# Optimization experiments

Measured on AMD Instinct MI355X. Metric: run time of the kernel, lower is better.

The kernel has to match this reference:

```python
import jax, jax.numpy as jnp
import numpy as np
import math

B, L, D_MODEL, H = 2, 2048, 2048, 16
HD = D_MODEL // H  # 128


def _rope(x):
    # x: (B,H,L,HD) interleaved-pair RoPE (GPT-NeoX / RoFormer style with ::2 strides)
    hd = x.shape[-1]
    inv_freq = 1.0 / (10000.0 ** (jnp.arange(0, hd, 2, dtype=jnp.float32) / hd))  # (HD/2,)
    t = jnp.arange(x.shape[2], dtype=jnp.float32)
    freqs = t[:, None] * inv_freq[None, :]            # (L, HD/2)
    cos = jnp.cos(freqs)[None, None]                  # (1,1,L,HD/2)
    sin = jnp.sin(freqs)[None, None]
    x1 = x[..., ::2]
    x2 = x[..., 1::2]
    even = x1 * cos - x2 * sin
    odd = x1 * sin + x2 * cos
    # interleave even/odd back: (...,HD/2,2) -> (...,HD)
    return jnp.stack([even, odd], axis=-1).reshape(x.shape)


def setup_inputs() -> dict:
    key = jax.random.key(0)
    k1, k2, k3, k4, k5, k6 = jax.random.split(key, 6)
    x_q = jax.random.normal(k1, (B, L, D_MODEL), dtype=jnp.float32)
    x_kv = jax.random.normal(k2, (B, L, D_MODEL), dtype=jnp.float32)
    # causal additive mask: 0 keep, -1e9 masked, broadcastable to (B,H,L,S)
    causal = jnp.tril(jnp.ones((L, L), dtype=bool))
    attn_mask = jnp.where(causal, 0.0, -1e9).astype(jnp.float32)[None, None]
    s = 0.02
    w_q = jax.random.normal(k3, (D_MODEL, D_MODEL), dtype=jnp.float32) * s
    w_k = jax.random.normal(k4, (D_MODEL, D_MODEL), dtype=jnp.float32) * s
    w_v = jax.random.normal(k5, (D_MODEL, D_MODEL), dtype=jnp.float32) * s
    w_o = jax.random.normal(k6, (D_MODEL, D_MODEL), dtype=jnp.float32) * s
    return {"x_q": x_q, "x_kv": x_kv, "attn_mask": attn_mask,
            "w_q": w_q, "w_k": w_k, "w_v": w_v, "w_o": w_o}


def _shape(x):
    b, l, _ = x.shape
    return x.reshape(b, l, H, HD).transpose(0, 2, 1, 3)  # (B,H,L,HD)


def reference(x_q, x_kv, attn_mask, w_q, w_k, w_v, w_o):
    # torch Linear (no bias): y = x @ W.T
    q = _shape(x_q @ w_q.T)
    k = _shape(x_kv @ w_k.T)
    v = _shape(x_kv @ w_v.T)
    q = _rope(q)
    k = _rope(k)
    scale = 1.0 / math.sqrt(HD)
    scores = jnp.einsum('bhld,bhsd->bhls', q, k) * scale + attn_mask
    attn = jax.nn.softmax(scores, axis=-1)            # (B,H,L,S)
    out = jnp.einsum('bhls,bhsd->bhld', attn, v)
    out = out.transpose(0, 2, 1, 3).reshape(x_q.shape[0], x_q.shape[1], H * HD)
    out = out @ w_o.T
    return (out, attn)
```

## Files before the change

kernel.cpp:

```cpp
#include <hip/hip_runtime.h>
#include <hip/hip_bf16.h>
#include <math.h>

#define B_ 2
#define L_ 2048
#define D_ 2048
#define H_ 16
#define HD_ 128
#define E_ (B_*L_*D_)
#define W_ (D_*D_)

typedef __bf16 bf16;
typedef __bf16 bf16x8 __attribute__((ext_vector_type(8)));
typedef __bf16 bf16x4 __attribute__((ext_vector_type(4)));
typedef float  f32x4  __attribute__((ext_vector_type(4)));

#define GLL16(gp_, lp_) __builtin_amdgcn_global_load_lds( \
    (const __attribute__((address_space(1))) void*)(gp_), \
    (__attribute__((address_space(3))) void*)(lp_), 16, 0, 0)

#define BARRIER() do { asm volatile("" ::: "memory"); \
    __builtin_amdgcn_s_barrier(); \
    asm volatile("" ::: "memory"); } while (0)

#define WAITN(N) asm volatile("s_waitcnt vmcnt(" #N ")" ::: "memory")
#define LGKM0SB() do { asm volatile("s_waitcnt lgkmcnt(0)" ::: "memory"); \
    __builtin_amdgcn_sched_barrier(0); } while (0)

__global__ void prep(const float* __restrict__ xq, const float* __restrict__ xkv,
                     const float* __restrict__ wq, const float* __restrict__ wk,
                     const float* __restrict__ wv, const float* __restrict__ wo,
                     bf16* __restrict__ xqb, bf16* __restrict__ xkvb,
                     bf16* __restrict__ wqb, bf16* __restrict__ wkb,
                     bf16* __restrict__ wvb, bf16* __restrict__ wob,
                     float* __restrict__ ct, float* __restrict__ st) {
  int g = blockIdx.x;
  if (g < 16384) {
    const float* s = (g < 8192) ? xq : xkv;
    bf16* d = (g < 8192) ? xqb : xkvb;
    int i = ((g & 8191) * 256 + threadIdx.x) * 4;
    f32x4 v = *reinterpret_cast<const f32x4*>(s + i);
    bf16x4 o; o[0]=(bf16)v[0]; o[1]=(bf16)v[1]; o[2]=(bf16)v[2]; o[3]=(bf16)v[3];
    *reinterpret_cast<bf16x4*>(d + i) = o;
  } else if (g < 32768) {
    int gg = g - 16384;
    int which = gg >> 12;
    const float* s = (which==0)?wq:(which==1)?wk:(which==2)?wv:wo;
    bf16* d = (which==0)?wqb:(which==1)?wkb:(which==2)?wvb:wob;
    int i = ((gg & 4095) * 256 + threadIdx.x) * 4;
    f32x4 v = *reinterpret_cast<const f32x4*>(s + i);
    bf16x4 o; o[0]=(bf16)v[0]; o[1]=(bf16)v[1]; o[2]=(bf16)v[2]; o[3]=(bf16)v[3];
    *reinterpret_cast<bf16x4*>(d + i) = o;
  } else {
    int idx = (g - 32768) * 256 + threadIdx.x;
    int t = idx >> 6, i = idx & 63;
    float inv = powf(10000.0f, -2.0f * (float)i / 128.0f);
    float f = (float)t * inv;
    ct[t * 64 + i] = cosf(f);
    st[t * 64 + i] = sinf(f);
  }
}

__global__ __launch_bounds__(512, 2) void gemm_qkv256(
    const bf16* __restrict__ xq, const bf16* __restrict__ xkv,
    const bf16* __restrict__ wq, const bf16* __restrict__ wk, const bf16* __restrict__ wv,
    const float* __restrict__ ct, const float* __restrict__ st,
    bf16* __restrict__ Qo, bf16* __restrict__ Ko, bf16* __restrict__ Vt) {
  __shared__ bf16 Ab[2][256 * 64];
  __shared__ bf16 Bb[2][256 * 64];
  const int tid = threadIdx.x;
  const int w = tid >> 6, lane = tid & 63;
  const int l15 = lane & 15, lg = lane >> 4;
  const int wm = w >> 2, wn = w & 3;
  const int which = blockIdx.x >> 3;
  const int n0 = (blockIdx.x & 7) * 256;
  const int m0 = blockIdx.y * 256;
  const bf16* A  = (which == 0) ? xq : xkv;
  const bf16* Wt = (which == 0) ? wq : ((which == 1) ? wk : wv);

  int rS[4], cS[4];
#pragma unroll
  for (int s = 0; s < 4; ++s) {
    int ch = s * 512 + tid;
    rS[s] = ch >> 3;
    cS[s] = ((ch & 7) ^ ((ch >> 3) & 7)) << 3;
  }

  auto stage = [&](int t, int buf) {
#pragma unroll
    for (int s = 0; s < 4; ++s) {
      GLL16(A  + (size_t)(m0 + rS[s]) * D_ + t * 64 + cS[s], &Ab[buf][0] + s * 4096 + w * 512);
      GLL16(Wt + (size_t)(n0 + rS[s]) * D_ + t * 64 + cS[s], &Bb[buf][0] + s * 4096 + w * 512);
    }
  };
#define RD(bufp, row, x) (*reinterpret_cast<const bf16x8*>((bufp) + (row) * 64 + (((x) ^ (l15 & 7)) << 3)))

  f32x4 acc[8][4];
#pragma unroll
  for (int i = 0; i < 8; ++i)
#pragma unroll
    for (int n = 0; n < 4; ++n) acc[i][n] = (f32x4){0.f, 0.f, 0.f, 0.f};

  stage(0, 0);
  WAITN(0);
  BARRIER();

  for (int t = 0; t < 32; ++t) {
    const bf16* Al = &Ab[t & 1][0];
    const bf16* Bl = &Bb[t & 1][0];
    bf16x8 af[4], bfr[4];
    const bool hn = (t + 1 < 32);

    if (hn) stage(t + 1, (t & 1) ^ 1);
#pragma unroll
    for (int n = 0; n < 4; ++n) bfr[n] = RD(Bl, wn * 64 + n * 16 + l15, lg);
#pragma unroll
    for (int i = 0; i < 4; ++i) af[i] = RD(Al, wm * 128 + i * 16 + l15, lg);
    BARRIER(); LGKM0SB();
    __builtin_amdgcn_s_setprio(1);
#pragma unroll
    for (int i = 0; i < 4; ++i)
#pragma unroll
      for (int n = 0; n < 4; ++n)
        acc[i][n] = __builtin_amdgcn_mfma_f32_16x16x32_bf16(af[i], bfr[n], acc[i][n], 0, 0, 0);
    __builtin_amdgcn_s_setprio(0);
    BARRIER();

#pragma unroll
    for (int i = 0; i < 4; ++i) af[i] = RD(Al, wm * 128 + (4 + i) * 16 + l15, lg);
    BARRIER(); LGKM0SB();
    __builtin_amdgcn_s_setprio(1);
#pragma unroll
    for (int i = 0; i < 4; ++i)
#pragma unroll
      for (int n = 0; n < 4; ++n)
        acc[4 + i][n] = __builtin_amdgcn_mfma_f32_16x16x32_bf16(af[i], bfr[n], acc[4 + i][n], 0, 0, 0);
    __builtin_amdgcn_s_setprio(0);
    BARRIER();

#pragma unroll
    for (int n = 0; n < 4; ++n) bfr[n] = RD(Bl, wn * 64 + n * 16 + l15, 4 + lg);
#pragma unroll
    for (int i = 0; i < 4; ++i) af[i] = RD(Al, wm * 128 + i * 16 + l15, 4 + lg);
    BARRIER(); LGKM0SB();
    __builtin_amdgcn_s_setprio(1);
#pragma unroll
    for (int i = 0; i < 4; ++i)
#pragma unroll
      for (int n = 0; n < 4; ++n)
        acc[i][n] = __builtin_amdgcn_mfma_f32_16x16x32_bf16(af[i], bfr[n], acc[i][n], 0, 0, 0);
    __builtin_amdgcn_s_setprio(0);
    BARRIER();

#pragma unroll
    for (int i = 0; i < 4; ++i) af[i] = RD(Al, wm * 128 + (4 + i) * 16 + l15, 4 + lg);
    BARRIER(); LGKM0SB();
    __builtin_amdgcn_s_setprio(1);
#pragma unroll
    for (int i = 0; i < 4; ++i)
#pragma unroll
      for (int n = 0; n < 4; ++n)
        acc[4 + i][n] = __builtin_amdgcn_mfma_f32_16x16x32_bf16(af[i], bfr[n], acc[4 + i][n], 0, 0, 0);
    __builtin_amdgcn_s_setprio(0);
    if (hn) WAITN(0);
    BARRIER();
  }
#undef RD

  if (which == 2) {
    const int b = m0 >> 11;
#pragma unroll
    for (int mi = 0; mi < 8; ++mi) {
      int row = m0 + wm * 128 + mi * 16 + lg * 4;
      int l = row & 2047;
#pragma unroll
      for (int ni = 0; ni < 4; ++ni) {
        int c = n0 + wn * 64 + ni * 16 + l15;
        int hd = (b * 16 + (c >> 7)) * 128 + (c & 127);
        bf16x4 o;
        o[0] = (bf16)acc[mi][ni][0]; o[1] = (bf16)acc[mi][ni][1];
        o[2] = (bf16)acc[mi][ni][2]; o[3] = (bf16)acc[mi][ni][3];
        *reinterpret_cast<bf16x4*>(Vt + (size_t)hd * L_ + l) = o;
      }
    }
  } else {
    bf16* Out = which ? Ko : Qo;
    const bool odd = (l15 & 1);
#pragma unroll
    for (int mi = 0; mi < 8; ++mi) {
      int row = m0 + wm * 128 + mi * 16 + lg * 4;
      int l = row & 2047;
#pragma unroll
      for (int ni = 0; ni < 4; ++ni) {
        int c = n0 + wn * 64 + ni * 16 + l15;
        int i = (c & 127) >> 1;
#pragma unroll
        for (int r = 0; r < 4; ++r) {
          float own = acc[mi][ni][r];
          float prt = __shfl_xor(own, 1, 64);
          float cc = ct[(size_t)(l + r) * 64 + i];
          float ss = st[(size_t)(l + r) * 64 + i];
          float res = odd ? (prt * ss + own * cc) : (own * cc - prt * ss);
          Out[(size_t)(row + r) * D_ + c] = (bf16)res;
        }
      }
    }
  }
}

__global__ __launch_bounds__(256, 4) void gemm_bt(const bf16* __restrict__ A,
                                                  const bf16* __restrict__ Bw,
                                                  float* __restrict__ Cout,
                                                  int M, int N, int K) {
  __shared__ bf16 As[128 * 64];
  __shared__ bf16 Bs[128 * 64];
  const int tid = threadIdx.x;
  const int lane = tid & 63;
  const int w = tid >> 6;
  const int l15 = lane & 15, lg = lane >> 4;
  const int m0 = blockIdx.y * 128, n0 = blockIdx.x * 128;
  const int wm = (w >> 1) * 64, wn = (w & 1) * 64;

  int rowS[4], schS[4];
#pragma unroll
  for (int s = 0; s < 4; ++s) {
    int cl = s * 256 + tid;
    rowS[s] = cl >> 3;
    schS[s] = ((cl & 7) ^ ((cl >> 3) & 7)) << 3;
  }

  f32x4 acc[4][4];
#pragma unroll
  for (int m = 0; m < 4; ++m)
#pragma unroll
    for (int n = 0; n < 4; ++n) acc[m][n] = (f32x4){0.f, 0.f, 0.f, 0.f};

  for (int kt = 0; kt < K; kt += 64) {
    __syncthreads();
#pragma unroll
    for (int s = 0; s < 4; ++s) {
      GLL16(A  + (size_t)(m0 + rowS[s]) * K + kt + schS[s], As + s * 2048 + w * 512);
      GLL16(Bw + (size_t)(n0 + rowS[s]) * K + kt + schS[s], Bs + s * 2048 + w * 512);
    }
    __syncthreads();
#pragma unroll
    for (int kk = 0; kk < 64; kk += 32) {
      bf16x8 af[4], bfr[4];
#pragma unroll
      for (int m = 0; m < 4; ++m)
        af[m] = *reinterpret_cast<const bf16x8*>(
            As + (wm + m * 16 + l15) * 64 + ((((kk >> 3) + lg) ^ (l15 & 7)) << 3));
#pragma unroll
      for (int n = 0; n < 4; ++n)
        bfr[n] = *reinterpret_cast<const bf16x8*>(
            Bs + (wn + n * 16 + l15) * 64 + ((((kk >> 3) + lg) ^ (l15 & 7)) << 3));
#pragma unroll
      for (int m = 0; m < 4; ++m)
#pragma unroll
        for (int n = 0; n < 4; ++n)
          acc[m][n] = __builtin_amdgcn_mfma_f32_16x16x32_bf16(af[m], bfr[n], acc[m][n], 0, 0, 0);
    }
  }
#pragma unroll
  for (int m = 0; m < 4; ++m) {
    int orow = m0 + wm + m * 16 + lg * 4;
#pragma unroll
    for (int n = 0; n < 4; ++n) {
      int col = n0 + wn + n * 16 + l15;
#pragma unroll
      for (int r = 0; r < 4; ++r)
        Cout[(size_t)(orow + r) * N + col] = acc[m][n][r];
    }
  }
}

__global__ __launch_bounds__(256, 2) void attn_fused(const bf16* __restrict__ Qb,
                                                     const bf16* __restrict__ Kb,
                                                     const bf16* __restrict__ Vt,
                                                     float* __restrict__ attn,
                                                     bf16* __restrict__ Oh) {
  __shared__ bf16 Klds[2][64 * 128];
  __shared__ bf16 Vlds[128 * 64];
  __shared__ bf16 Plds[4][32][72];

  const int tid = threadIdx.x;
  const int w = tid >> 6, lane = tid & 63;
  const int l15 = lane & 15, lg = lane >> 4;

  int g = blockIdx.x + 16 * blockIdx.y;
  int tq, bh;
  if (g < 256) { tq = g & 15;  bh = g >> 4; }
  else { int h2 = g - 256; tq = 15 - (h2 & 15); bh = 16 + (h2 >> 4); }
  const int b = bh >> 4, h = bh & 15;

  const int q0w = tq * 128 + w * 32;
  const int ntW = (q0w >> 6) + 1;
  const int ntB = 2 * tq + 2;
  const float sc2 = 0.08838834764831845f * 1.44269504088896f;

  const bf16* kb = Kb + ((size_t)b * L_) * D_ + h * HD_;
  const bf16* vb = Vt + (size_t)bh * HD_ * L_;
  float* arow = attn + ((size_t)bh * L_ + q0w) * L_;

  bf16x8 qf[2][4];
#pragma unroll
  for (int qc = 0; qc < 2; ++qc) {
    const bf16* qrow = Qb + ((size_t)b * L_ + q0w + qc * 16 + l15) * D_ + h * HD_;
#pragma unroll
    for (int c = 0; c < 4; ++c)
      qf[qc][c] = *reinterpret_cast<const bf16x8*>(qrow + c * 32 + lg * 8);
  }

  int rK[4], sK[4], rV[4], sV[4];
#pragma unroll
  for (int s = 0; s < 4; ++s) {
    int ck = s * 256 + tid;
    rK[s] = ck >> 4; sK[s] = ((ck & 15) ^ (rK[s] & 7)) << 3;
    rV[s] = ck >> 3; sV[s] = ((ck & 7) ^ (rV[s] & 7)) << 3;
  }

  auto stageK = [&](int gp, int buf) {
#pragma unroll
    for (int s = 0; s < 4; ++s)
      GLL16(kb + (size_t)(gp * 64 + rK[s]) * D_ + sK[s],
            &Klds[0][0] + buf * 8192 + s * 2048 + w * 512);
  };
  auto stageV = [&](int gp) {
#pragma unroll
    for (int s = 0; s < 4; ++s)
      GLL16(vb + (size_t)rV[s] * L_ + gp * 64 + sV[s],
            Vlds + s * 2048 + w * 512);
  };
  auto qkt = [&](const bf16* kl, f32x4 acc[2][4]) {
#pragma unroll
    for (int c = 0; c < 4; ++c)
#pragma unroll
      for (int t = 0; t < 4; ++t) {
        bf16x8 kf = *reinterpret_cast<const bf16x8*>(
            kl + (t * 16 + l15) * 128 + ((((c << 2) + lg) ^ (l15 & 7)) << 3));
#pragma unroll
        for (int qc = 0; qc < 2; ++qc)
          acc[qc][t] = __builtin_amdgcn_mfma_f32_16x16x32_bf16(qf[qc][c], kf, acc[qc][t], 0, 0, 0);
      }
  };
  auto zstore32 = [&](int gp) {
#pragma unroll
    for (int qc = 0; qc < 2; ++qc)
#pragma unroll
      for (int t = 0; t < 4; ++t)
#pragma unroll
        for (int r = 0; r < 4; ++r)
          arow[(size_t)(qc * 16 + lg * 4 + r) * L_ + gp * 64 + t * 16 + l15] = 0.f;
  };

  float sum[2][4] = {{0.f,0.f,0.f,0.f},{0.f,0.f,0.f,0.f}};
  stageK(0, 0);
  for (int gp = 0; gp < ntB; ++gp) {
    BARRIER();
    const bool hn = (gp + 1 < ntB);
    if (hn) { stageK(gp + 1, (gp + 1) & 1); WAITN(4); }
    else    { WAITN(0); }
    BARRIER();
    if (gp < ntW) {
      f32x4 acc[2][4];
#pragma unroll
      for (int qc = 0; qc < 2; ++qc)
#pragma unroll
        for (int t = 0; t < 4; ++t) acc[qc][t] = (f32x4){0.f,0.f,0.f,0.f};
      qkt(&Klds[gp & 1][0], acc);
      if (gp < ntW - 1) {
#pragma unroll
        for (int qc = 0; qc < 2; ++qc)
#pragma unroll
          for (int t = 0; t < 4; ++t)
#pragma unroll
            for (int r = 0; r < 4; ++r)
              sum[qc][r] += exp2f(acc[qc][t][r] * sc2);
      } else {
#pragma unroll
        for (int qc = 0; qc < 2; ++qc)
#pragma unroll
          for (int t = 0; t < 4; ++t)
#pragma unroll
            for (int r = 0; r < 4; ++r) {
              int kc = gp * 64 + t * 16 + l15;
              int qr = q0w + qc * 16 + lg * 4 + r;
              sum[qc][r] += (kc <= qr) ? exp2f(acc[qc][t][r] * sc2) : 0.f;
            }
      }
    } else {
      zstore32(gp);
    }
  }
  float rinv[2][4];
#pragma unroll
  for (int qc = 0; qc < 2; ++qc)
#pragma unroll
    for (int r = 0; r < 4; ++r) {
      float s = sum[qc][r];
#pragma unroll
      for (int sh = 1; sh < 16; sh <<= 1)
        s += __shfl_xor(s, sh, 64);
      rinv[qc][r] = 1.0f / s;
    }

  f32x4 oacc[2][8];
#pragma unroll
  for (int qc = 0; qc < 2; ++qc)
#pragma unroll
    for (int i = 0; i < 8; ++i) oacc[qc][i] = (f32x4){0.f, 0.f, 0.f, 0.f};

  BARRIER();
  stageK(0, 0);
  for (int gp = 0; gp < ntB; ++gp) {
    BARRIER();
    stageV(gp);
    const bool hn = (gp + 1 < ntB);
    if (hn) stageK(gp + 1, (gp + 1) & 1);
    if (gp == 0) { WAITN(8); }
    else if (hn) { WAITN(40); }
    else         { WAITN(36); }
    BARRIER();
    const bool act = gp < ntW;
    float pv[2][4][4];
    if (act) {
      f32x4 acc[2][4];
#pragma unroll
      for (int qc = 0; qc < 2; ++qc)
#pragma unroll
        for (int t = 0; t < 4; ++t) acc[qc][t] = (f32x4){0.f,0.f,0.f,0.f};
      qkt(&Klds[gp & 1][0], acc);
      if (gp < ntW - 1) {
#pragma unroll
        for (int qc = 0; qc < 2; ++qc)
#pragma unroll
          for (int t = 0; t < 4; ++t)
#pragma unroll
            for (int r = 0; r < 4; ++r)
              pv[qc][t][r] = exp2f(acc[qc][t][r] * sc2) * rinv[qc][r];
      } else {
#pragma unroll
        for (int qc = 0; qc < 2; ++qc)
#pragma unroll
          for (int t = 0; t < 4; ++t)
#pragma unroll
            for (int r = 0; r < 4; ++r) {
              int kc = gp * 64 + t * 16 + l15;
              int qr = q0w + qc * 16 + lg * 4 + r;
              pv[qc][t][r] = (kc <= qr) ? exp2f(acc[qc][t][r] * sc2) * rinv[qc][r] : 0.f;
            }
      }
#pragma unroll
      for (int qc = 0; qc < 2; ++qc)
#pragma unroll
        for (int t = 0; t < 4; ++t)
#pragma unroll
          for (int r = 0; r < 4; ++r)
            Plds[w][qc * 16 + lg * 4 + r][t * 16 + l15] = (bf16)pv[qc][t][r];
    }
    if (hn) WAITN(4); else WAITN(0);
    if (act) {
#pragma unroll
      for (int qc = 0; qc < 2; ++qc)
#pragma unroll
        for (int t = 0; t < 4; ++t)
#pragma unroll
          for (int r = 0; r < 4; ++r)
            arow[(size_t)(qc * 16 + lg * 4 + r) * L_ + gp * 64 + t * 16 + l15] = pv[qc][t][r];
    } else {
      zstore32(gp);
    }
    BARRIER();
    if (act) {
      asm volatile("s_waitcnt lgkmcnt(0)" ::: "memory");
      __builtin_amdgcn_sched_barrier(0);
      bf16x8 pa[2][2];
#pragma unroll
      for (int qc = 0; qc < 2; ++qc)
#pragma unroll
        for (int ck = 0; ck < 2; ++ck)
          pa[qc][ck] = *reinterpret_cast<const bf16x8*>(&Plds[w][qc * 16 + l15][ck * 32 + lg * 8]);
#pragma unroll
      for (int ck = 0; ck < 2; ++ck)
#pragma unroll
        for (int t8 = 0; t8 < 8; ++t8) {
          bf16x8 vf = *reinterpret_cast<const bf16x8*>(
              Vlds + (t8 * 16 + l15) * 64 + ((((ck << 2) + lg) ^ (l15 & 7)) << 3));
#pragma unroll
          for (int qc = 0; qc < 2; ++qc)
            oacc[qc][t8] = __builtin_amdgcn_mfma_f32_16x16x32_bf16(pa[qc][ck], vf, oacc[qc][t8], 0, 0, 0);
        }
      asm volatile("s_waitcnt lgkmcnt(0)" ::: "memory");
    }
  }

  for (int gp2 = ntB; gp2 < 32; ++gp2) {
#pragma unroll
    for (int i = 0; i < 8; ++i)
      *reinterpret_cast<f32x4*>(arow + (size_t)(i * 4 + lg) * L_ + gp2 * 64 + l15 * 4)
          = (f32x4){0.f, 0.f, 0.f, 0.f};
  }

#pragma unroll
  for (int qc = 0; qc < 2; ++qc) {
    bf16* orow = Oh + ((size_t)b * L_ + q0w + qc * 16) * D_ + h * HD_;
#pragma unroll
    for (int t8 = 0; t8 < 8; ++t8)
#pragma unroll
      for (int r = 0; r < 4; ++r)
        orow[(size_t)(lg * 4 + r) * D_ + t8 * 16 + l15] = (bf16)oacc[qc][t8][r];
  }
}

extern "C" void kernel_launch(void* const* d_in, const int* in_sizes, int n_in,
                              void* d_out, int out_size, void* d_ws, size_t ws_size,
                              hipStream_t stream) {
  const float* x_q  = (const float*)d_in[0];
  const float* x_kv = (const float*)d_in[1];
  const float* w_q = (const float*)d_in[3];
  const float* w_k = (const float*)d_in[4];
  const float* w_v = (const float*)d_in[5];
  const float* w_o = (const float*)d_in[6];

  char* p = (char*)d_ws;
  auto alloc = [&](size_t bytes) { char* r = p; p += (bytes + 255) & ~(size_t)255; return r; };
  bf16* xq_b  = (bf16*)alloc((size_t)E_ * 2);
  bf16* xkv_b = (bf16*)alloc((size_t)E_ * 2);
  bf16* wq_b  = (bf16*)alloc((size_t)W_ * 2);
  bf16* wk_b  = (bf16*)alloc((size_t)W_ * 2);
  bf16* wv_b  = (bf16*)alloc((size_t)W_ * 2);
  bf16* wo_b  = (bf16*)alloc((size_t)W_ * 2);
  bf16* Qraw  = (bf16*)alloc((size_t)E_ * 2);
  bf16* Kraw  = (bf16*)alloc((size_t)E_ * 2);
  bf16* Vt    = (bf16*)alloc((size_t)E_ * 2);
  bf16* Oh    = (bf16*)alloc((size_t)E_ * 2);
  float* ct   = (float*)alloc((size_t)L_ * 64 * 4);
  float* st2  = (float*)alloc((size_t)L_ * 64 * 4);

  float* out0     = (float*)d_out;
  float* attn_out = out0 + E_;

  prep<<<33280, 256, 0, stream>>>(x_q, x_kv, w_q, w_k, w_v, w_o,
                                  xq_b, xkv_b, wq_b, wk_b, wv_b, wo_b, ct, st2);
  gemm_qkv256<<<dim3(24, 16), 512, 0, stream>>>(xq_b, xkv_b, wq_b, wk_b, wv_b,
                                                ct, st2, Qraw, Kraw, Vt);
  attn_fused<<<dim3(16, 32), 256, 0, stream>>>(Qraw, Kraw, Vt, attn_out, Oh);
  gemm_bt<<<dim3(16, 32), 256, 0, stream>>>(Oh, wo_b, out0, B_*L_, D_, D_);
}
```

Measured before the change: 456.3 us.

## Restructure QKV GEMM to 128x256 tiles with triple-buffered LDS pipeline

The QKV projection GEMM moves from 256x256 tiles with double buffering to 128x256 tiles with a three-stage LDS ring. The next-next K tile is prefetched and its loads are split across two compute phases, with partial vmcnt waits. Smaller M tiles double the grid from 384 to 768 blocks to improve CU fill on the 256-CU device, and fewer barriers run per K step. The cost is more LDS per block, which may limit co-residency, and less A/B reuse per tile.

```diff
diff --git a/kernel.cpp b/kernel.cpp
--- a/kernel.cpp
+++ b/kernel.cpp
@@ -61,142 +61,138 @@
   }
 }
 
-__global__ __launch_bounds__(512, 2) void gemm_qkv256(
+__global__ __launch_bounds__(512, 2) void gemm_qkv8p(
     const bf16* __restrict__ xq, const bf16* __restrict__ xkv,
     const bf16* __restrict__ wq, const bf16* __restrict__ wk, const bf16* __restrict__ wv,
     const float* __restrict__ ct, const float* __restrict__ st,
     bf16* __restrict__ Qo, bf16* __restrict__ Ko, bf16* __restrict__ Vt) {
-  __shared__ bf16 Ab[2][256 * 64];
-  __shared__ bf16 Bb[2][256 * 64];
+  __shared__ bf16 Ab[3][128 * 64];
+  __shared__ bf16 Bb[3][256 * 64];
   const int tid = threadIdx.x;
   const int w = tid >> 6, lane = tid & 63;
   const int l15 = lane & 15, lg = lane >> 4;
   const int wm = w >> 2, wn = w & 3;
   const int which = blockIdx.x >> 3;
   const int n0 = (blockIdx.x & 7) * 256;
-  const int m0 = blockIdx.y * 256;
+  const int m0 = blockIdx.y * 128;
   const bf16* A  = (which == 0) ? xq : xkv;
   const bf16* Wt = (which == 0) ? wq : ((which == 1) ? wk : wv);
 
-  int rS[4], cS[4];
+  int rA[2], cA[2], rB[4], cB[4];
+#pragma unroll
+  for (int s = 0; s < 2; ++s) {
+    int ch = s * 512 + tid; rA[s] = ch >> 3; cA[s] = ((ch & 7) ^ (rA[s] & 7)) << 3;
+  }
 #pragma unroll
   for (int s = 0; s < 4; ++s) {
-    int ch = s * 512 + tid;
-    rS[s] = ch >> 3;
-    cS[s] = ((ch & 7) ^ ((ch >> 3) & 7)) << 3;
-  }
-
-  auto stage = [&](int t, int buf) {
-#pragma unroll
-    for (int s = 0; s < 4; ++s) {
-      GLL16(A  + (size_t)(m0 + rS[s]) * D_ + t * 64 + cS[s], &Ab[buf][0] + s * 4096 + w * 512);
-      GLL16(Wt + (size_t)(n0 + rS[s]) * D_ + t * 64 + cS[s], &Bb[buf][0] + s * 4096 + w * 512);
-    }
+    int ch = s * 512 + tid; rB[s] = ch >> 3; cB[s] = ((ch & 7) ^ (rB[s] & 7)) << 3;
+  }
+  auto stageA = [&](int t, int buf, int s) {
+    GLL16(A + (size_t)(m0 + rA[s]) * D_ + t * 64 + cA[s], &Ab[buf][0] + s * 4096 + w * 512);
   };
-#define RD(bufp, row, x) (*reinterpret_cast<const bf16x8*>((bufp) + (row) * 64 + (((x) ^ (l15 & 7)) << 3)))
-
-  f32x4 acc[8][4];
-#pragma unroll
-  for (int i = 0; i < 8; ++i)
-#pragma unroll
-    for (int n = 0; n < 4; ++n) acc[i][n] = (f32x4){0.f, 0.f, 0.f, 0.f};
-
-  stage(0, 0);
-  WAITN(0);
+  auto stageB = [&](int t, int buf, int s) {
+    GLL16(Wt + (size_t)(n0 + rB[s]) * D_ + t * 64 + cB[s], &Bb[buf][0] + s * 4096 + w * 512);
+  };
+#define RDS(bufp, R, x) (*reinterpret_cast<const bf16x8*>((bufp) + (R) * 64 + (((x) ^ ((R) & 7)) << 3)))
+
+  f32x4 acc[4][4];
+#pragma unroll
+  for (int i = 0; i < 4; ++i)
+#pragma unroll
+    for (int j = 0; j < 4; ++j) acc[i][j] = (f32x4){0.f, 0.f, 0.f, 0.f};
+
+#pragma unroll
+  for (int s = 0; s < 2; ++s) stageA(0, 0, s);
+#pragma unroll
+  for (int s = 0; s < 4; ++s) stageB(0, 0, s);
+#pragma unroll
+  for (int s = 0; s < 2; ++s) stageA(1, 1, s);
+#pragma unroll
+  for (int s = 0; s < 4; ++s) stageB(1, 1, s);
+  WAITN(6);
   BARRIER();
 
+  bf16x8 afr[4][2];
   for (int t = 0; t < 32; ++t) {
-    const bf16* Al = &Ab[t & 1][0];
-    const bf16* Bl = &Bb[t & 1][0];
-    bf16x8 af[4], bfr[4];
-    const bool hn = (t + 1 < 32);
-
-    if (hn) stage(t + 1, (t & 1) ^ 1);
-#pragma unroll
-    for (int n = 0; n < 4; ++n) bfr[n] = RD(Bl, wn * 64 + n * 16 + l15, lg);
-#pragma unroll
-    for (int i = 0; i < 4; ++i) af[i] = RD(Al, wm * 128 + i * 16 + l15, lg);
+    const bf16* Al = &Ab[t % 3][0];
+    const bf16* Bl = &Bb[t % 3][0];
+    const int nb = (t + 2) % 3;
+    const bool stg = (t + 2 < 32);
+    bf16x8 bfr[2][2];
+
+#pragma unroll
+    for (int fr = 0; fr < 4; ++fr)
+#pragma unroll
+      for (int ks = 0; ks < 2; ++ks)
+        afr[fr][ks] = RDS(Al, wm * 64 + fr * 16 + l15, ks * 4 + lg);
+#pragma unroll
+    for (int fc = 0; fc < 2; ++fc)
+#pragma unroll
+      for (int ks = 0; ks < 2; ++ks)
+        bfr[fc][ks] = RDS(Bl, wn * 64 + fc * 16 + l15, ks * 4 + lg);
+    if (stg) { stageA(t + 2, nb, 0); stageA(t + 2, nb, 1); stageB(t + 2, nb, 0); }
     BARRIER(); LGKM0SB();
     __builtin_amdgcn_s_setprio(1);
 #pragma unroll
-    for (int i = 0; i < 4; ++i)
-#pragma unroll
-      for (int n = 0; n < 4; ++n)
-        acc[i][n] = __builtin_amdgcn_mfma_f32_16x16x32_bf16(af[i], bfr[n], acc[i][n], 0, 0, 0);
+    for (int fr = 0; fr < 4; ++fr)
+#pragma unroll
+      for (int fc = 0; fc < 2; ++fc)
+#pragma unroll
+        for (int ks = 0; ks < 2; ++ks)
+          acc[fr][fc] = __builtin_amdgcn_mfma_f32_16x16x32_bf16(afr[fr][ks], bfr[fc][ks], acc[fr][fc], 0, 0, 0);
     __builtin_amdgcn_s_setprio(0);
     BARRIER();
 
 #pragma unroll
-    for (int i = 0; i < 4; ++i) af[i] = RD(Al, wm * 128 + (4 + i) * 16 + l15, lg);
+    for (int fc = 0; fc < 2; ++fc)
+#pragma unroll
+      for (int ks = 0; ks < 2; ++ks)
+        bfr[fc][ks] = RDS(Bl, wn * 64 + (2 + fc) * 16 + l15, ks * 4 + lg);
+    if (stg) { stageB(t + 2, nb, 1); stageB(t + 2, nb, 2); stageB(t + 2, nb, 3); }
     BARRIER(); LGKM0SB();
     __builtin_amdgcn_s_setprio(1);
 #pragma unroll
-    for (int i = 0; i < 4; ++i)
-#pragma unroll
-      for (int n = 0; n < 4; ++n)
-        acc[4 + i][n] = __builtin_amdgcn_mfma_f32_16x16x32_bf16(af[i], bfr[n], acc[4 + i][n], 0, 0, 0);
+    for (int fr = 0; fr < 4; ++fr)
+#pragma unroll
+      for (int fc = 0; fc < 2; ++fc)
+#pragma unroll
+        for (int ks = 0; ks < 2; ++ks)
+          acc[fr][2 + fc] = __builtin_amdgcn_mfma_f32_16x16x32_bf16(afr[fr][ks], bfr[fc][ks], acc[fr][2 + fc], 0, 0, 0);
     __builtin_amdgcn_s_setprio(0);
-    BARRIER();
-
-#pragma unroll
-    for (int n = 0; n < 4; ++n) bfr[n] = RD(Bl, wn * 64 + n * 16 + l15, 4 + lg);
-#pragma unroll
-    for (int i = 0; i < 4; ++i) af[i] = RD(Al, wm * 128 + i * 16 + l15, 4 + lg);
-    BARRIER(); LGKM0SB();
-    __builtin_amdgcn_s_setprio(1);
-#pragma unroll
-    for (int i = 0; i < 4; ++i)
-#pragma unroll
-      for (int n = 0; n < 4; ++n)
-        acc[i][n] = __builtin_amdgcn_mfma_f32_16x16x32_bf16(af[i], bfr[n], acc[i][n], 0, 0, 0);
-    __builtin_amdgcn_s_setprio(0);
-    BARRIER();
-
-#pragma unroll
-    for (int i = 0; i < 4; ++i) af[i] = RD(Al, wm * 128 + (4 + i) * 16 + l15, 4 + lg);
-    BARRIER(); LGKM0SB();
-    __builtin_amdgcn_s_setprio(1);
-#pragma unroll
-    for (int i = 0; i < 4; ++i)
-#pragma unroll
-      for (int n = 0; n < 4; ++n)
-        acc[4 + i][n] = __builtin_amdgcn_mfma_f32_16x16x32_bf16(af[i], bfr[n], acc[4 + i][n], 0, 0, 0);
-    __builtin_amdgcn_s_setprio(0);
-    if (hn) WAITN(0);
-    BARRIER();
-  }
-#undef RD
+    if (t < 30) { if (stg) WAITN(6); else WAITN(0); }
+    BARRIER();
+  }
+#undef RDS
 
   if (which == 2) {
     const int b = m0 >> 11;
 #pragma unroll
-    for (int mi = 0; mi < 8; ++mi) {
-      int row = m0 + wm * 128 + mi * 16 + lg * 4;
-      int l = row & 2047;
-#pragma unroll
-      for (int ni = 0; ni < 4; ++ni) {
-        int c = n0 + wn * 64 + ni * 16 + l15;
+    for (int fr = 0; fr < 4; ++fr) {
+      int l0 = (m0 & 2047) + wm * 64 + fr * 16 + lg * 4;
+#pragma unroll
+      for (int fc = 0; fc < 4; ++fc) {
+        int c = n0 + wn * 64 + fc * 16 + l15;
         int hd = (b * 16 + (c >> 7)) * 128 + (c & 127);
         bf16x4 o;
-        o[0] = (bf16)acc[mi][ni][0]; o[1] = (bf16)acc[mi][ni][1];
-        o[2] = (bf16)acc[mi][ni][2]; o[3] = (bf16)acc[mi][ni][3];
-        *reinterpret_cast<bf16x4*>(Vt + (size_t)hd * L_ + l) = o;
+        o[0] = (bf16)acc[fr][fc][0]; o[1] = (bf16)acc[fr][fc][1];
+        o[2] = (bf16)acc[fr][fc][2]; o[3] = (bf16)acc[fr][fc][3];
+        *reinterpret_cast<bf16x4*>(Vt + (size_t)hd * L_ + l0) = o;
       }
     }
   } else {
     bf16* Out = which ? Ko : Qo;
     const bool odd = (l15 & 1);
 #pragma unroll
-    for (int mi = 0; mi < 8; ++mi) {
-      int row = m0 + wm * 128 + mi * 16 + lg * 4;
+    for (int fr = 0; fr < 4; ++fr) {
+      int row = m0 + wm * 64 + fr * 16 + lg * 4;
       int l = row & 2047;
 #pragma unroll
-      for (int ni = 0; ni < 4; ++ni) {
-        int c = n0 + wn * 64 + ni * 16 + l15;
+      for (int fc = 0; fc < 4; ++fc) {
+        int c = n0 + wn * 64 + fc * 16 + l15;
         int i = (c & 127) >> 1;
 #pragma unroll
         for (int r = 0; r < 4; ++r) {
-          float own = acc[mi][ni][r];
+          float own = acc[fr][fc][r];
           float prt = __shfl_xor(own, 1, 64);
           float cc = ct[(size_t)(l + r) * 64 + i];
           float ss = st[(size_t)(l + r) * 64 + i];
@@ -542,8 +538,8 @@
 
   prep<<<33280, 256, 0, stream>>>(x_q, x_kv, w_q, w_k, w_v, w_o,
                                   xq_b, xkv_b, wq_b, wk_b, wv_b, wo_b, ct, st2);
-  gemm_qkv256<<<dim3(24, 16), 512, 0, stream>>>(xq_b, xkv_b, wq_b, wk_b, wv_b,
-                                                ct, st2, Qraw, Kraw, Vt);
+  gemm_qkv8p<<<dim3(24, 32), 512, 0, stream>>>(xq_b, xkv_b, wq_b, wk_b, wv_b,
+                                               ct, st2, Qraw, Kraw, Vt);
   attn_fused<<<dim3(16, 32), 256, 0, stream>>>(Qraw, Kraw, Vt, attn_out, Oh);
   gemm_bt<<<dim3(16, 32), 256, 0, stream>>>(Oh, wo_b, out0, B_*L_, D_, D_);
 }
```

New measurement: 409.3 us. 10.3% less time.
